# Optimization experiments

Hardware: AMD Instinct MI355X
Metric: run time of the kernel (lower is better)

## Reference

```python
import jax, jax.numpy as jnp
import numpy as np

B, T, C = 4, 2048, 1024
NH = 16
HD = C // NH  # 64


def setup_inputs() -> dict:
    key = jax.random.key(0)
    k1, k2, k3, k4, k5 = jax.random.split(key, 5)
    s_in = 1.0 / np.sqrt(C)
    return {
        "x": jax.random.normal(k1, (B, T, C), dtype=jnp.float32),
        "attention_mask": jnp.ones((B, T), dtype=jnp.float32),
        "W_qkv": jax.random.normal(k2, (C, 3 * C), dtype=jnp.float32) * s_in,
        "b_qkv": jnp.zeros((3 * C,), dtype=jnp.float32),
        "W_out": jax.random.normal(k3, (C, C), dtype=jnp.float32) * s_in,
        "b_out": jnp.zeros((C,), dtype=jnp.float32),
    }


def reference(x, attention_mask, W_qkv, b_qkv, W_out, b_out):
    Bx, Tx, Cx = x.shape
    # QKV projection: (B,T,3C)
    qkv = x @ W_qkv + b_qkv
    Q, K, V = jnp.split(qkv, 3, axis=-1)
    # (B, NH, T, HD)
    Q = Q.reshape(Bx, Tx, NH, HD).transpose(0, 2, 1, 3)
    K = K.reshape(Bx, Tx, NH, HD).transpose(0, 2, 1, 3)
    V = V.reshape(Bx, Tx, NH, HD).transpose(0, 2, 1, 3)
    # scaled scores (B, NH, T, T)
    scores = jnp.einsum("bhqd,bhkd->bhqk", Q, K) * (1.0 / np.sqrt(HD))
    # causal mask: set strictly-upper triangle to -inf (mask-fill semantics)
    causal = jnp.tril(jnp.ones((Tx, Tx), dtype=bool))[None, None]
    scores = jnp.where(causal, scores, -jnp.inf)
    # additive padding mask
    pad = (1.0 - attention_mask)[:, None, None, :] * jnp.finfo(scores.dtype).min
    scores = scores + pad
    attn = jax.nn.softmax(scores, axis=-1)
    # weighted values -> (B, T, C)
    wv = jnp.einsum("bhqk,bhkd->bhqd", attn, V)
    wv = wv.transpose(0, 2, 1, 3).reshape(Bx, Tx, Cx)
    return wv @ W_out + b_out
```

## Files before the change

### kernel.cpp

```cpp
#include <hip/hip_runtime.h>
#include <math.h>

constexpr int BB = 4;
constexpr int TT = 2048;
constexpr int CC = 1024;
constexpr int NHH = 16;
constexpr int HDD = 64;
constexpr int C3 = 3 * CC;

typedef __bf16 bf16x8 __attribute__((ext_vector_type(8)));
typedef float  f32x4  __attribute__((ext_vector_type(4)));

__device__ __forceinline__ unsigned short f2bf(float x) {
    union { float f; unsigned u; } v; v.f = x;
    unsigned r = v.u + 0x7fffu + ((v.u >> 16) & 1u);
    return (unsigned short)(r >> 16);
}

#define AS1(p) ((const __attribute__((address_space(1))) void*)(p))
#define AS3(p) ((__attribute__((address_space(3))) void*)(p))

constexpr float SM2 = 17.312340490667561f;

constexpr int CAST_BLOCKS = (BB * TT * CC / 4) / 256;
constexpr int TQKV_BLOCKS = (C3 / 64) * (CC / 64);
constexpr int TOUT_BLOCKS = (CC / 64) * (CC / 64);
constexpr int KB_BLOCKS   = (BB * TT) / 256;

__global__ __launch_bounds__(256) void prep(
    const float* __restrict__ x,
    const float* __restrict__ Wqkv,
    const float* __restrict__ Wout,
    const float* __restrict__ amask,
    unsigned short* __restrict__ xb,
    unsigned short* __restrict__ Wqkvt,
    unsigned short* __restrict__ Woutt,
    float* __restrict__ kbias)
{
    __shared__ float tile[64][65];
    const int bid = blockIdx.x;
    const int t = threadIdx.x;

    if (bid < CAST_BLOCKS) {
        const int i = bid * 256 + t;
        float4 v = ((const float4*)x)[i];
        ushort4 o;
        o.x = f2bf(v.x); o.y = f2bf(v.y); o.z = f2bf(v.z); o.w = f2bf(v.w);
        ((ushort4*)xb)[i] = o;
        return;
    }
    if (bid >= CAST_BLOCKS + TQKV_BLOCKS + TOUT_BLOCKS) {
        const int i = (bid - CAST_BLOCKS - TQKV_BLOCKS - TOUT_BLOCKS) * 256 + t;
        kbias[i] = (amask[i] - 1.0f) * 1.0e38f - SM2;
        return;
    }

    const float* src; unsigned short* dst; int R, Cn, r0, c0;
    if (bid < CAST_BLOCKS + TQKV_BLOCKS) {
        const int tb = bid - CAST_BLOCKS;
        src = Wqkv; dst = Wqkvt; R = CC; Cn = C3;
        c0 = (tb % (C3 / 64)) * 64; r0 = (tb / (C3 / 64)) * 64;
    } else {
        const int tb = bid - CAST_BLOCKS - TQKV_BLOCKS;
        src = Wout; dst = Woutt; R = CC; Cn = CC;
        c0 = (tb % (CC / 64)) * 64; r0 = (tb / (CC / 64)) * 64;
    }

    const int lr = t >> 4, lc = (t & 15) * 4;
    #pragma unroll
    for (int s = 0; s < 4; ++s) {
        float4 v = *(const float4*)&src[(size_t)(r0 + lr + s * 16) * Cn + c0 + lc];
        tile[lr + s * 16][lc + 0] = v.x;
        tile[lr + s * 16][lc + 1] = v.y;
        tile[lr + s * 16][lc + 2] = v.z;
        tile[lr + s * 16][lc + 3] = v.w;
    }
    __syncthreads();
    const int oi = t >> 2, oc = (t & 3) * 16;
    unsigned short buf[16];
    #pragma unroll
    for (int u = 0; u < 16; ++u)
        buf[u] = f2bf(tile[oc + u][oi]);
    unsigned short* d = &dst[(size_t)(c0 + oi) * R + r0 + oc];
    *(uint4*)(d + 0) = *(uint4*)&buf[0];
    *(uint4*)(d + 8) = *(uint4*)&buf[8];
}

template<bool VSPLIT>
__global__ __launch_bounds__(256) void gemm_bt_mfma(
    const unsigned short* __restrict__ A,
    const unsigned short* __restrict__ Bt,
    const float* __restrict__ bias,
    float* __restrict__ OutF,
    unsigned short* __restrict__ Qp,
    unsigned short* __restrict__ Kp,
    unsigned short* __restrict__ Vtp,
    int M, int N, int K, float qscale)
{
    __shared__ alignas(16) unsigned short As[128 * 64];
    __shared__ alignas(16) unsigned short Bs[128 * 64];

    const int tid  = threadIdx.x;
    const int w    = tid >> 6;
    const int lane = tid & 63;
    const int quad = lane >> 4;
    const int col  = lane & 15;
    const int m0 = blockIdx.y * 128, n0 = blockIdx.x * 128;
    const int wr = w >> 1, wc = w & 1;

    f32x4 acc[4][4];
    #pragma unroll
    for (int i = 0; i < 4; ++i)
        #pragma unroll
        for (int j = 0; j < 4; ++j)
            #pragma unroll
            for (int r = 0; r < 4; ++r)
                acc[i][j][r] = 0.0f;

    const int srow = tid >> 3;
    const int spos = tid & 7;
    char* AsB = (char*)As;
    char* BsB = (char*)Bs;

    for (int k0 = 0; k0 < K; k0 += 64) {
        if (k0) __syncthreads();
        #pragma unroll
        for (int i = 0; i < 4; ++i) {
            const int row = srow + 32 * i;
            const int sch = spos ^ (row & 7);
            __builtin_amdgcn_global_load_lds(
                AS1(A + (size_t)(m0 + row) * K + k0 + sch * 8),
                AS3(AsB + i * 4096 + w * 1024), 16, 0, 0);
            __builtin_amdgcn_global_load_lds(
                AS1(Bt + (size_t)(n0 + row) * K + k0 + sch * 8),
                AS3(BsB + i * 4096 + w * 1024), 16, 0, 0);
        }
        __syncthreads();

        #pragma unroll
        for (int ks = 0; ks < 2; ++ks) {
            bf16x8 af[4], bf[4];
            #pragma unroll
            for (int i = 0; i < 4; ++i) {
                const int ra = wr * 64 + i * 16 + col;
                const int pa = ((quad + ks * 4) ^ (ra & 7)) * 8;
                af[i] = *(const bf16x8*)&As[ra * 64 + pa];
                const int rb = wc * 64 + i * 16 + col;
                const int pb = ((quad + ks * 4) ^ (rb & 7)) * 8;
                bf[i] = *(const bf16x8*)&Bs[rb * 64 + pb];
            }
            #pragma unroll
            for (int i = 0; i < 4; ++i)
                #pragma unroll
                for (int j = 0; j < 4; ++j)
                    acc[i][j] = __builtin_amdgcn_mfma_f32_16x16x32_bf16(af[i], bf[j], acc[i][j], 0, 0, 0);
        }
    }

    if (VSPLIT) {
        if (n0 < CC) {
            #pragma unroll
            for (int i = 0; i < 4; ++i)
                #pragma unroll
                for (int r = 0; r < 4; ++r) {
                    const int m = m0 + wr * 64 + i * 16 + quad * 4 + r;
                    #pragma unroll
                    for (int j = 0; j < 4; ++j) {
                        const int n = n0 + wc * 64 + j * 16 + col;
                        Qp[(size_t)m * CC + n] = f2bf((acc[i][j][r] + bias[n]) * qscale);
                    }
                }
        } else if (n0 < 2 * CC) {
            #pragma unroll
            for (int i = 0; i < 4; ++i) {
                const int mb   = m0 + wr * 64 + i * 16 + quad * 4;
                const int bidx = mb >> 11;
                const int tloc = mb & 2047;
                #pragma unroll
                for (int j = 0; j < 4; ++j) {
                    const int n  = n0 + wc * 64 + j * 16 + col;
                    const int hh = (n - CC) >> 6;
                    const int dd = (n - CC) & 63;
                    #pragma unroll
                    for (int r = 0; r < 4; ++r)
                        Kp[(((size_t)bidx * NHH + hh) * TT + tloc + r) * HDD + dd] =
                            f2bf(acc[i][j][r] + bias[n]);
                }
            }
        } else {
            #pragma unroll
            for (int i = 0; i < 4; ++i) {
                const int mb   = m0 + wr * 64 + i * 16 + quad * 4;
                const int bidx = mb >> 11;
                const int tloc = mb & 2047;
                const int ktile = tloc >> 6, tc = tloc & 63;
                #pragma unroll
                for (int j = 0; j < 4; ++j) {
                    const int n  = n0 + wc * 64 + j * 16 + col;
                    const int hh = (n - 2 * CC) >> 6;
                    const int dd = (n - 2 * CC) & 63;
                    unsigned short pk[4];
                    #pragma unroll
                    for (int r = 0; r < 4; ++r)
                        pk[r] = f2bf(acc[i][j][r] + bias[n]);
                    *(uint2*)&Vtp[((((size_t)bidx * NHH + hh) * 32 + ktile) * HDD + dd) * 64 + tc] =
                        *(const uint2*)pk;
                }
            }
        }
    } else {
        #pragma unroll
        for (int i = 0; i < 4; ++i)
            #pragma unroll
            for (int r = 0; r < 4; ++r) {
                const int m = m0 + wr * 64 + i * 16 + quad * 4 + r;
                #pragma unroll
                for (int j = 0; j < 4; ++j) {
                    const int n = n0 + wc * 64 + j * 16 + col;
                    OutF[(size_t)m * N + n] = acc[i][j][r] + bias[n];
                }
            }
    }
}

constexpr int PP = 72;

__global__ __launch_bounds__(256, 3) void attn_mfma(
    const unsigned short* __restrict__ Qp,
    const unsigned short* __restrict__ Kp,
    const unsigned short* __restrict__ Vtp,
    const float* __restrict__ kbias,
    unsigned short* __restrict__ WV)
{
    __shared__ alignas(16) unsigned short Ks [2][64 * 64];
    __shared__ alignas(16) unsigned short Vts[2][64 * 64];
    __shared__ alignas(16) __bf16        Ps[4][32 * PP];

    const int tid  = threadIdx.x;
    const int w    = tid >> 6;
    const int lane = tid & 63;
    const int quad = lane >> 4;
    const int col  = lane & 15;

    const int gi = blockIdx.x;
    const int j  = gi >> 3;
    const int bh = ((gi & 7) << 3) | (j & 7);
    const int qb = 15 - (j >> 3);
    const int b = bh >> 4, h = bh & 15;

    const unsigned short* Qg = Qp + (size_t)b * TT * CC + (size_t)h * HDD;
    const unsigned short* Kg = Kp + (size_t)bh * TT * HDD;
    const unsigned short* Vg = Vtp + (size_t)bh * 32 * HDD * 64;
    const float* kb_g = kbias + b * TT;

    const int srow = tid >> 3;
    const int sch  = (tid & 7) ^ (srow & 7);
    char* KsB  = (char*)&Ks[0][0];
    char* VtsB = (char*)&Vts[0][0];

    const int qw = qb * 128 + w * 32;
    const int ntiles = 2 * qb + 2;

    bf16x8 qfa0 = *(const bf16x8*)(Qg + (size_t)(qw + col) * CC + quad * 8);
    bf16x8 qfa1 = *(const bf16x8*)(Qg + (size_t)(qw + col) * CC + 32 + quad * 8);
    bf16x8 qfb0 = *(const bf16x8*)(Qg + (size_t)(qw + 16 + col) * CC + quad * 8);
    bf16x8 qfb1 = *(const bf16x8*)(Qg + (size_t)(qw + 16 + col) * CC + 32 + quad * 8);

    f32x4 o[2][4];
    float l[2][4];
    #pragma unroll
    for (int hh = 0; hh < 2; ++hh)
        #pragma unroll
        for (int t = 0; t < 4; ++t)
            #pragma unroll
            for (int r = 0; r < 4; ++r) o[hh][t][r] = 0.0f;
    #pragma unroll
    for (int hh = 0; hh < 2; ++hh)
        #pragma unroll
        for (int r = 0; r < 4; ++r) l[hh][r] = 0.0f;

    auto DMA = [&](int tile, int buf) {
        #pragma unroll
        for (int i = 0; i < 2; ++i) {
            __builtin_amdgcn_global_load_lds(
                AS1(Kg + (size_t)(tile * 64 + srow + 32 * i) * HDD + sch * 8),
                AS3(KsB + buf * 8192 + i * 4096 + w * 1024), 16, 0, 0);
            __builtin_amdgcn_global_load_lds(
                AS1(Vg + ((size_t)tile * 64 + srow + 32 * i) * 64 + sch * 8),
                AS3(VtsB + buf * 8192 + i * 4096 + w * 1024), 16, 0, 0);
        }
    };

    float kbc[4], kbn[4];
    DMA(0, 0);
    #pragma unroll
    for (int t = 0; t < 4; ++t) kbc[t] = kb_g[t * 16 + col];
    DMA(1, 1);
    #pragma unroll
    for (int t = 0; t < 4; ++t) kbn[t] = kb_g[64 + t * 16 + col];
    asm volatile("s_waitcnt vmcnt(8)" ::: "memory");
    __builtin_amdgcn_s_barrier();

    for (int it = 0; it < ntiles; ++it) {
        const int kt  = it << 6;
        const int cur = it & 1;

        if (kt <= qw + 31) {
            const unsigned short* ksb = &Ks[cur][0];
            const unsigned short* vsb = &Vts[cur][0];

            f32x4 s[2][4];
            #pragma unroll
            for (int t = 0; t < 4; ++t) {
                const int row = t * 16 + col;
                const int c0 = (quad ^ (row & 7)) * 8;
                const int c1 = ((quad + 4) ^ (row & 7)) * 8;
                bf16x8 k0 = *(const bf16x8*)&ksb[row * 64 + c0];
                bf16x8 k1 = *(const bf16x8*)&ksb[row * 64 + c1];
                f32x4 z;
                #pragma unroll
                for (int r = 0; r < 4; ++r) z[r] = kbc[t];
                f32x4 za = __builtin_amdgcn_mfma_f32_16x16x32_bf16(qfa0, k0, z, 0, 0, 0);
                za = __builtin_amdgcn_mfma_f32_16x16x32_bf16(qfa1, k1, za, 0, 0, 0);
                s[0][t] = za;
                f32x4 zb = __builtin_amdgcn_mfma_f32_16x16x32_bf16(qfb0, k0, z, 0, 0, 0);
                zb = __builtin_amdgcn_mfma_f32_16x16x32_bf16(qfb1, k1, zb, 0, 0, 0);
                s[1][t] = zb;
            }

            const bool needc = (kt + 64 > qw);
            #pragma unroll
            for (int hh = 0; hh < 2; ++hh)
                #pragma unroll
                for (int t = 0; t < 4; ++t) {
                    const int key = kt + t * 16 + col;
                    #pragma unroll
                    for (int r = 0; r < 4; ++r) {
                        float p = __builtin_amdgcn_exp2f(s[hh][t][r]);
                        if (needc && key > qw + hh * 16 + quad * 4 + r) p = 0.0f;
                        l[hh][r] += p;
                        Ps[w][(hh * 16 + quad * 4 + r) * PP + t * 16 + col] = (__bf16)p;
                    }
                }

            bf16x8 p0a = *(const bf16x8*)&Ps[w][col * PP + quad * 8];
            bf16x8 p1a = *(const bf16x8*)&Ps[w][col * PP + 32 + quad * 8];
            bf16x8 p0b = *(const bf16x8*)&Ps[w][(16 + col) * PP + quad * 8];
            bf16x8 p1b = *(const bf16x8*)&Ps[w][(16 + col) * PP + 32 + quad * 8];
            #pragma unroll
            for (int t = 0; t < 4; ++t) {
                const int row = t * 16 + col;
                const int c0 = (quad ^ (row & 7)) * 8;
                const int c1 = ((quad + 4) ^ (row & 7)) * 8;
                bf16x8 v0 = *(const bf16x8*)&vsb[row * 64 + c0];
                bf16x8 v1 = *(const bf16x8*)&vsb[row * 64 + c1];
                o[0][t] = __builtin_amdgcn_mfma_f32_16x16x32_bf16(p0a, v0, o[0][t], 0, 0, 0);
                o[0][t] = __builtin_amdgcn_mfma_f32_16x16x32_bf16(p1a, v1, o[0][t], 0, 0, 0);
                o[1][t] = __builtin_amdgcn_mfma_f32_16x16x32_bf16(p0b, v0, o[1][t], 0, 0, 0);
                o[1][t] = __builtin_amdgcn_mfma_f32_16x16x32_bf16(p1b, v1, o[1][t], 0, 0, 0);
            }
        }

        __builtin_amdgcn_s_barrier();

        #pragma unroll
        for (int t = 0; t < 4; ++t) kbc[t] = kbn[t];

        if (it + 2 < ntiles) {
            DMA(it + 2, cur);
            #pragma unroll
            for (int t = 0; t < 4; ++t)
                kbn[t] = kb_g[(it + 2) * 64 + t * 16 + col];
            asm volatile("s_waitcnt vmcnt(8)" ::: "memory");
        } else {
            asm volatile("s_waitcnt vmcnt(0)" ::: "memory");
        }
        __builtin_amdgcn_s_barrier();
    }

    #pragma unroll
    for (int hh = 0; hh < 2; ++hh) {
        #pragma unroll
        for (int off = 1; off < 16; off <<= 1)
            #pragma unroll
            for (int r = 0; r < 4; ++r)
                l[hh][r] += __shfl_xor(l[hh][r], off);
        #pragma unroll
        for (int r = 0; r < 4; ++r) {
            const float inv = 1.0f / l[hh][r];
            const int q = qw + hh * 16 + quad * 4 + r;
            unsigned short* dst = WV + ((size_t)b * TT + q) * CC + (size_t)h * HDD;
            #pragma unroll
            for (int t = 0; t < 4; ++t)
                dst[t * 16 + col] = f2bf(o[hh][t][r] * inv);
        }
    }
}

extern "C" void kernel_launch(void* const* d_in, const int* in_sizes, int n_in,
                              void* d_out, int out_size, void* d_ws, size_t ws_size,
                              hipStream_t stream) {
    const float* x     = (const float*)d_in[0];
    const float* amask = (const float*)d_in[1];
    const float* Wqkv  = (const float*)d_in[2];
    const float* bqkv  = (const float*)d_in[3];
    const float* Wout  = (const float*)d_in[4];
    const float* bout  = (const float*)d_in[5];
    float* out = (float*)d_out;

    const int M = BB * TT;

    unsigned short* xb    = (unsigned short*)d_ws;
    unsigned short* Wqkvt = xb    + (size_t)M * CC;
    unsigned short* Woutt = Wqkvt + (size_t)C3 * CC;
    unsigned short* Qp    = Woutt + (size_t)CC * CC;
    unsigned short* Kp    = Qp    + (size_t)M * CC;
    unsigned short* Vtp   = Kp    + (size_t)M * CC;
    unsigned short* wvb   = Vtp   + (size_t)M * CC;
    float*          kbias = (float*)(wvb + (size_t)M * CC);

    dim3 blk(256);

    prep<<<dim3(CAST_BLOCKS + TQKV_BLOCKS + TOUT_BLOCKS + KB_BLOCKS), blk, 0, stream>>>(
        x, Wqkv, Wout, amask, xb, Wqkvt, Woutt, kbias);

    gemm_bt_mfma<true><<<dim3(C3 / 128, M / 128), blk, 0, stream>>>(
        xb, Wqkvt, bqkv, nullptr, Qp, Kp, Vtp, M, C3, CC, 0.18033688011112043f);
    attn_mfma<<<dim3(1024), dim3(256), 0, stream>>>(
        Qp, Kp, Vtp, kbias, wvb);
    gemm_bt_mfma<false><<<dim3(CC / 128, M / 128), blk, 0, stream>>>(
        wvb, Woutt, bout, out, nullptr, nullptr, nullptr, M, CC, CC, 1.0f);
}
```

Before: 243.7 us.

## Double-buffer GEMM LDS tiles with async prefetch and swizzled block order

Converts the bf16 MFMA GEMM main loop to use two LDS buffers. Tile kt+2 is loaded directly into LDS while tile kt+1 is ready, and the wait is controlled with explicit vmcnt waits and barriers. It also remaps block indices into 8-wide M-groups to improve L2 reuse, and sets launch bounds to 2 blocks per CU. This hides global load latency behind MFMA work, at the cost of doubled LDS (64KB per block) and fragile hand-written waitcnt logic. The remap hardcodes 64 M-tiles, which may not match every GEMM shape that uses this kernel.

```diff
diff --git a/kernel.cpp b/kernel.cpp
--- a/kernel.cpp
+++ b/kernel.cpp
@@ -87,7 +87,7 @@
 }
 
 template<bool VSPLIT>
-__global__ __launch_bounds__(256) void gemm_bt_mfma(
+__global__ __launch_bounds__(256, 2) void gemm_bt_mfma(
     const unsigned short* __restrict__ A,
     const unsigned short* __restrict__ Bt,
     const float* __restrict__ bias,
@@ -97,15 +97,21 @@
     unsigned short* __restrict__ Vtp,
     int M, int N, int K, float qscale)
 {
-    __shared__ alignas(16) unsigned short As[128 * 64];
-    __shared__ alignas(16) unsigned short Bs[128 * 64];
+    __shared__ alignas(16) unsigned short As[2][128 * 64];
+    __shared__ alignas(16) unsigned short Bs[2][128 * 64];
 
     const int tid  = threadIdx.x;
     const int w    = tid >> 6;
     const int lane = tid & 63;
     const int quad = lane >> 4;
     const int col  = lane & 15;
-    const int m0 = blockIdx.y * 128, n0 = blockIdx.x * 128;
+
+    const int nX  = gridDim.x;
+    const int lin = blockIdx.y * nX + blockIdx.x;
+    const int pos = lin >> 3;
+    const int mt  = ((lin & 7) << 3) | (pos & 7);
+    const int nt  = pos >> 3;
+    const int m0 = mt * 128, n0 = nt * 128;
     const int wr = w >> 1, wc = w & 1;
 
     f32x4 acc[4][4];
@@ -119,23 +125,35 @@
 
     const int srow = tid >> 3;
     const int spos = tid & 7;
-    char* AsB = (char*)As;
-    char* BsB = (char*)Bs;
-
-    for (int k0 = 0; k0 < K; k0 += 64) {
-        if (k0) __syncthreads();
+    char* AsB = (char*)&As[0][0];
+    char* BsB = (char*)&Bs[0][0];
+
+    const int nk = K >> 6;
+
+    auto DMA = [&](int kt, int buf) {
+        const int k0 = kt << 6;
         #pragma unroll
         for (int i = 0; i < 4; ++i) {
             const int row = srow + 32 * i;
             const int sch = spos ^ (row & 7);
             __builtin_amdgcn_global_load_lds(
                 AS1(A + (size_t)(m0 + row) * K + k0 + sch * 8),
-                AS3(AsB + i * 4096 + w * 1024), 16, 0, 0);
+                AS3(AsB + buf * 16384 + i * 4096 + w * 1024), 16, 0, 0);
             __builtin_amdgcn_global_load_lds(
                 AS1(Bt + (size_t)(n0 + row) * K + k0 + sch * 8),
-                AS3(BsB + i * 4096 + w * 1024), 16, 0, 0);
-        }
-        __syncthreads();
+                AS3(BsB + buf * 16384 + i * 4096 + w * 1024), 16, 0, 0);
+        }
+    };
+
+    DMA(0, 0);
+    DMA(1, 1);
+    asm volatile("s_waitcnt vmcnt(8)" ::: "memory");
+    __builtin_amdgcn_s_barrier();
+
+    for (int kt = 0; kt < nk; ++kt) {
+        const int cur = kt & 1;
+        const unsigned short* as = &As[cur][0];
+        const unsigned short* bs = &Bs[cur][0];
 
         #pragma unroll
         for (int ks = 0; ks < 2; ++ks) {
@@ -144,10 +162,10 @@
             for (int i = 0; i < 4; ++i) {
                 const int ra = wr * 64 + i * 16 + col;
                 const int pa = ((quad + ks * 4) ^ (ra & 7)) * 8;
-                af[i] = *(const bf16x8*)&As[ra * 64 + pa];
+                af[i] = *(const bf16x8*)&as[ra * 64 + pa];
                 const int rb = wc * 64 + i * 16 + col;
                 const int pb = ((quad + ks * 4) ^ (rb & 7)) * 8;
-                bf[i] = *(const bf16x8*)&Bs[rb * 64 + pb];
+                bf[i] = *(const bf16x8*)&bs[rb * 64 + pb];
             }
             #pragma unroll
             for (int i = 0; i < 4; ++i)
@@ -155,6 +173,15 @@
                 for (int j = 0; j < 4; ++j)
                     acc[i][j] = __builtin_amdgcn_mfma_f32_16x16x32_bf16(af[i], bf[j], acc[i][j], 0, 0, 0);
         }
+
+        __builtin_amdgcn_s_barrier();
+        if (kt + 2 < nk) {
+            DMA(kt + 2, cur);
+            asm volatile("s_waitcnt vmcnt(8)" ::: "memory");
+        } else {
+            asm volatile("s_waitcnt vmcnt(0)" ::: "memory");
+        }
+        __builtin_amdgcn_s_barrier();
     }
 
     if (VSPLIT) {
```

Result: faster. 238.1 us (-2.3%).
